# Kernel optimization log

Hardware: AMD Instinct MI355X
Metric: run time of the kernel (lower is better)

Reference implementation:

```python
import jax, jax.numpy as jnp
import numpy as np

N, F_IN, H1, H2, E = 100000, 256, 128, 64, 1600000


def _glorot(key, shape):
    lim = np.sqrt(6.0 / (shape[0] + shape[1]))
    return jax.random.uniform(key, shape, jnp.float32, -lim, lim)


def setup_inputs() -> dict:
    key = jax.random.key(0)
    ks = jax.random.split(key, 8)
    x = jax.random.normal(ks[0], (N, F_IN), jnp.float32)
    edge_index = jax.random.randint(ks[1], (2, E), 0, N, jnp.int64)
    return {
        "x": x,
        "w1": _glorot(ks[2], (F_IN, H1)),
        "b1": jnp.zeros((H1,), jnp.float32),
        "w2": _glorot(ks[3], (H1, H2)),
        "b2": jnp.zeros((H2,), jnp.float32),
        "w3": _glorot(ks[4], (H1, H2)),
        "b3": jnp.zeros((H2,), jnp.float32),
        "edge_index": edge_index,
    }


def _gcn_conv(x, w, b, src, dst, dinv_sqrt):
    # GCNConv: transform first, then symmetric-normalized aggregation with self-loops.
    h = x @ w                                   # [N, out]
    coef = dinv_sqrt[src] * dinv_sqrt[dst]      # [E]
    agg = jnp.zeros_like(h).at[dst].add(h[src] * coef[:, None])
    # self-loop contribution: coefficient deg^-1 per node
    agg = agg + h * (dinv_sqrt * dinv_sqrt)[:, None]
    return agg + b


def reference(x, w1, b1, w2, b2, w3, b3, edge_index):
    src, dst = edge_index[0], edge_index[1]
    n = x.shape[0]
    # degree including self-loop (edge weights all 1)
    deg = jnp.ones((n,), x.dtype).at[dst].add(1.0)
    dinv_sqrt = jax.lax.rsqrt(deg)
    hidden = jax.nn.relu(_gcn_conv(x, w1, b1, src, dst, dinv_sqrt))
    mu = _gcn_conv(hidden, w2, b2, src, dst, dinv_sqrt)
    logvar = _gcn_conv(hidden, w3, b3, src, dst, dinv_sqrt)
    return (mu, logvar)
```

## Files before the change

### kernel.cpp

```cpp
#include <hip/hip_runtime.h>


#define TPB 256
#define GSHIFT 9
#define GSIZE 512
#define PART_M 4096

typedef __attribute__((ext_vector_type(8))) short short8;
typedef __attribute__((ext_vector_type(4))) short short4v;
typedef __attribute__((ext_vector_type(4))) float floatx4;
typedef __attribute__((ext_vector_type(4))) unsigned int uint4v;

__device__ __forceinline__ void split2(float v, short& hi, short& lo) {
    unsigned u = __float_as_uint(v);
    float hf = __uint_as_float(u & 0xFFFF0000u);
    float lf = v - hf;
    hi = (short)(u >> 16);
    lo = (short)(__float_as_uint(lf) >> 16);
}

__device__ __forceinline__ short bf16_rtn(float v) {
    unsigned u = __float_as_uint(v);
    u += 0x7FFF + ((u >> 16) & 1);
    return (short)(u >> 16);
}

__device__ __forceinline__ void addrow(float* a, uint4v v) {
    a[0] += __uint_as_float(v[0] << 16); a[1] += __uint_as_float(v[0] & 0xFFFF0000u);
    a[2] += __uint_as_float(v[1] << 16); a[3] += __uint_as_float(v[1] & 0xFFFF0000u);
    a[4] += __uint_as_float(v[2] << 16); a[5] += __uint_as_float(v[2] & 0xFFFF0000u);
    a[6] += __uint_as_float(v[3] << 16); a[7] += __uint_as_float(v[3] & 0xFFFF0000u);
}

__device__ __forceinline__ void gather_accum(float* acc, const int* __restrict__ csr,
                                             int start, int deg, const uint4v* hp,
                                             int l16) {
    for (int jj = 0; jj < deg; jj += 16) {
        int rem = deg - jj;
        if (rem > 16) rem = 16;
        int il = (l16 < rem) ? l16 : rem - 1;
        int myIdx = csr[start + jj + il];
        int r = 0;
        for (; r + 3 < rem; r += 4) {
            int i0 = __shfl(myIdx, r + 0, 16);
            int i1 = __shfl(myIdx, r + 1, 16);
            int i2 = __shfl(myIdx, r + 2, 16);
            int i3 = __shfl(myIdx, r + 3, 16);
            uint4v v0 = hp[(size_t)i0 * 16 + l16];
            uint4v v1 = hp[(size_t)i1 * 16 + l16];
            uint4v v2 = hp[(size_t)i2 * 16 + l16];
            uint4v v3 = hp[(size_t)i3 * 16 + l16];
            addrow(acc, v0);
            addrow(acc, v1);
            addrow(acc, v2);
            addrow(acc, v3);
        }
        for (; r < rem; ++r) {
            int i = __shfl(myIdx, r, 16);
            addrow(acc, hp[(size_t)i * 16 + l16]);
        }
    }
}

__device__ __forceinline__ void gload_lds16(const void* g, void* l) {
    __builtin_amdgcn_global_load_lds(
        (const __attribute__((address_space(1))) unsigned int*)g,
        (__attribute__((address_space(3))) unsigned int*)l, 16, 0, 0);
}

__global__ __launch_bounds__(TPB) void prep_all(const float* __restrict__ w1,
                                                const float* __restrict__ w2,
                                                const float* __restrict__ b2,
                                                const float* __restrict__ w3,
                                                const float* __restrict__ b3,
                                                short* __restrict__ w1t_h,
                                                short* __restrict__ w1t_l,
                                                short* __restrict__ wct_h,
                                                short* __restrict__ wct_l,
                                                float* __restrict__ bcat,
                                                int* __restrict__ cursor) {
    int b = blockIdx.x, t0 = threadIdx.x;
    if (b < 128) {
        int t = b * TPB + t0;
        int k = t & 255, n = t >> 8;
        float v = w1[(size_t)k * 128 + n];
        short h, l;
        split2(v, h, l);
        w1t_h[t] = h;
        w1t_l[t] = l;
    } else if (b < 192) {
        int t = (b - 128) * TPB + t0;
        int k = t & 127, n = t >> 7;
        float v = (n < 64) ? w2[(size_t)k * 64 + n] : w3[(size_t)k * 64 + (n - 64)];
        short h, l;
        split2(v, h, l);
        wct_h[t] = h;
        wct_l[t] = l;
        if (t < 64) { bcat[t] = b2[t]; bcat[64 + t] = b3[t]; }
    } else {
        for (int i = t0; i < 513; i += TPB) cursor[i] = 0;
    }
}

__global__ __launch_bounds__(TPB) void group_count(const int* __restrict__ dst,
                                                   int* __restrict__ cursor, int E) {
    int* ghist = cursor;
    int* done  = cursor + 512;
    int* goff  = cursor + 513;
    __shared__ int h[256];
    __shared__ int lastFlag;
    int t = threadIdx.x;
    h[t] = 0;
    __syncthreads();
    const int4* d4 = (const int4*)dst;
    int E4 = E >> 2;
    int stride = gridDim.x * TPB;
    for (int k = blockIdx.x * TPB + t; k < E4; k += stride) {
        int4 v = d4[k];
        atomicAdd(&h[v.x >> GSHIFT], 1);
        atomicAdd(&h[v.y >> GSHIFT], 1);
        atomicAdd(&h[v.z >> GSHIFT], 1);
        atomicAdd(&h[v.w >> GSHIFT], 1);
    }
    for (int k = (E4 << 2) + blockIdx.x * TPB + t; k < E; k += stride)
        atomicAdd(&h[dst[k] >> GSHIFT], 1);
    __syncthreads();
    if (h[t]) atomicAdd(&ghist[t], h[t]);
    __threadfence();
    __syncthreads();
    if (t == 0) lastFlag = (atomicAdd(done, 1) == (int)gridDim.x - 1);
    __syncthreads();
    if (!lastFlag) return;
    int v = atomicAdd(&ghist[t], 0);
    h[t] = v;
    __syncthreads();
#pragma unroll
    for (int off = 1; off < 256; off <<= 1) {
        int x = (t >= off) ? h[t - off] : 0;
        __syncthreads();
        h[t] += x;
        __syncthreads();
    }
    goff[t] = h[t] - v;
    if (t == 255) goff[256] = h[255];
}

__global__ __launch_bounds__(256) void partition_kernel(const int* __restrict__ src,
                                                        const int* __restrict__ dst,
                                                        const int* __restrict__ goff,
                                                        int* __restrict__ gcur,
                                                        int* __restrict__ staged, int E) {
    __shared__ int sc[256];
    __shared__ int cur[256];
    __shared__ int gb[256];
    int t = threadIdx.x;
    int base = blockIdx.x * PART_M;
    int mloc = min(PART_M, E - base);
    int m4 = mloc >> 2;

    sc[t] = 0;
    cur[t] = 0;
    __syncthreads();
    const int4* d4 = (const int4*)(dst + base);
    const int4* s4 = (const int4*)(src + base);
    for (int k = t; k < m4; k += 256) {
        int4 v = d4[k];
        atomicAdd(&sc[v.x >> GSHIFT], 1);
        atomicAdd(&sc[v.y >> GSHIFT], 1);
        atomicAdd(&sc[v.z >> GSHIFT], 1);
        atomicAdd(&sc[v.w >> GSHIFT], 1);
    }
    for (int k = (m4 << 2) + t; k < mloc; k += 256)
        atomicAdd(&sc[dst[base + k] >> GSHIFT], 1);
    __syncthreads();
    int v = sc[t];
    gb[t] = v ? goff[t] + atomicAdd(&gcur[t], v) : 0;
    __syncthreads();
    for (int k = t; k < m4; k += 256) {
        int4 dv = d4[k];
        int4 sv = s4[k];
        int b0 = dv.x >> GSHIFT;
        staged[gb[b0] + atomicAdd(&cur[b0], 1)] = (sv.x << GSHIFT) | (dv.x & (GSIZE - 1));
        int b1 = dv.y >> GSHIFT;
        staged[gb[b1] + atomicAdd(&cur[b1], 1)] = (sv.y << GSHIFT) | (dv.y & (GSIZE - 1));
        int b2 = dv.z >> GSHIFT;
        staged[gb[b2] + atomicAdd(&cur[b2], 1)] = (sv.z << GSHIFT) | (dv.z & (GSIZE - 1));
        int b3 = dv.w >> GSHIFT;
        staged[gb[b3] + atomicAdd(&cur[b3], 1)] = (sv.w << GSHIFT) | (dv.w & (GSIZE - 1));
    }
    for (int k = (m4 << 2) + t; k < mloc; k += 256) {
        int d = dst[base + k];
        int s = src[base + k];
        int b = d >> GSHIFT;
        staged[gb[b] + atomicAdd(&cur[b], 1)] = (s << GSHIFT) | (d & (GSIZE - 1));
    }
}

__global__ __launch_bounds__(512) void build_csr(const int* __restrict__ staged,
                                                 const int* __restrict__ goff,
                                                 int* __restrict__ cnt,
                                                 float* __restrict__ dinv,
                                                 int* __restrict__ rowptr,
                                                 int* __restrict__ csr, int N) {
    __shared__ int hist[512];
    __shared__ int sc[512];
    __shared__ int lrow[512];
    __shared__ int cur[512];
    int t = threadIdx.x;
    int g = blockIdx.x;
    int s0 = goff[g], s1 = goff[g + 1];
    hist[t] = 0;
    cur[t] = 0;
    __syncthreads();
    for (int k = s0 + t; k < s1; k += 512)
        atomicAdd(&hist[staged[k] & (GSIZE - 1)], 1);
    __syncthreads();
    int v = hist[t];
    sc[t] = v;
    __syncthreads();
#pragma unroll
    for (int off = 1; off < 512; off <<= 1) {
        int x = (t >= off) ? sc[t - off] : 0;
        __syncthreads();
        sc[t] += x;
        __syncthreads();
    }
    int rp = s0 + sc[t] - v;
    lrow[t] = rp;
    int node = (g << GSHIFT) + t;
    if (node < N) {
        rowptr[node] = rp;
        cnt[node] = v;
        dinv[node] = rsqrtf(1.0f + (float)v);
    }
    __syncthreads();
    for (int k = s0 + t; k < s1; k += 512) {
        int p = staged[k];
        int dl = p & (GSIZE - 1);
        int pos = lrow[dl] + atomicAdd(&cur[dl], 1);
        csr[pos] = p >> GSHIFT;
    }
}

__global__ __launch_bounds__(TPB) void gemm_mfma_f32in(const float* __restrict__ A,
                                                       const short* __restrict__ Bth,
                                                       const short* __restrict__ Btl,
                                                       const float* __restrict__ rs,
                                                       short* __restrict__ Cb, int M, int K) {
    __shared__ float Af[2][64 * 32];
    __shared__ short Bh[2][128 * 32];
    __shared__ short Bl[2][128 * 32];
    int t = threadIdx.x;
    int wave = t >> 6, lane = t & 63, quad = lane >> 4, l16 = lane & 15;
    int bm0 = blockIdx.x * 64;

    floatx4 acc[8];
#pragma unroll
    for (int nt = 0; nt < 8; ++nt) acc[nt] = (floatx4){0.f, 0.f, 0.f, 0.f};

    auto stage = [&](int pb, int k0) {
#pragma unroll
        for (int i = 0; i < 2; ++i) {
            int g = i * 256 + t;
            int row = g >> 3, col = g & 7;
            int gr = bm0 + row;
            if (gr >= M) gr = M - 1;
            int scol = col ^ (row & 7);
            gload_lds16(A + (size_t)gr * K + k0 + scol * 4,
                        &Af[pb][(i * 256 + wave * 64) * 4]);
        }
#pragma unroll
        for (int i = 0; i < 2; ++i) {
            int g = i * 256 + t;
            int row = g >> 2, col = g & 3;
            int scol = col ^ ((row >> 1) & 3);
            size_t off = (size_t)row * K + k0 + scol * 8;
            int lb = (i * 256 + wave * 64) * 8;
            gload_lds16(Bth + off, &Bh[pb][lb]);
            gload_lds16(Btl + off, &Bl[pb][lb]);
        }
    };

    int nk = K >> 5;
    stage(0, 0);
    __syncthreads();
    int am = wave * 16 + l16;
    int ac0 = ((quad * 2 + 0) ^ (am & 7)) * 4;
    int ac1 = ((quad * 2 + 1) ^ (am & 7)) * 4;
    int bc = (quad ^ ((l16 >> 1) & 3)) * 8;
    for (int ks = 0; ks < nk; ++ks) {
        int pb = ks & 1;
        if (ks + 1 < nk) stage(pb ^ 1, (ks + 1) << 5);
        float4 fa0 = *(const float4*)&Af[pb][am * 32 + ac0];
        float4 fa1 = *(const float4*)&Af[pb][am * 32 + ac1];
        short8 a_h, a_l;
        {
            short h, l;
            split2(fa0.x, h, l); a_h[0] = h; a_l[0] = l;
            split2(fa0.y, h, l); a_h[1] = h; a_l[1] = l;
            split2(fa0.z, h, l); a_h[2] = h; a_l[2] = l;
            split2(fa0.w, h, l); a_h[3] = h; a_l[3] = l;
            split2(fa1.x, h, l); a_h[4] = h; a_l[4] = l;
            split2(fa1.y, h, l); a_h[5] = h; a_l[5] = l;
            split2(fa1.z, h, l); a_h[6] = h; a_l[6] = l;
            split2(fa1.w, h, l); a_h[7] = h; a_l[7] = l;
        }
#pragma unroll
        for (int nt = 0; nt < 8; ++nt) {
            int bn = nt * 16 + l16;
            short8 b_h = *(const short8*)&Bh[pb][bn * 32 + bc];
            short8 b_l = *(const short8*)&Bl[pb][bn * 32 + bc];
            acc[nt] = __builtin_amdgcn_mfma_f32_16x16x32_bf16(a_l, b_h, acc[nt], 0, 0, 0);
            acc[nt] = __builtin_amdgcn_mfma_f32_16x16x32_bf16(a_h, b_l, acc[nt], 0, 0, 0);
            acc[nt] = __builtin_amdgcn_mfma_f32_16x16x32_bf16(a_h, b_h, acc[nt], 0, 0, 0);
        }
        __syncthreads();
    }
#pragma unroll
    for (int reg = 0; reg < 4; ++reg) {
        int gr = bm0 + wave * 16 + quad * 4 + reg;
        if (gr < M) {
            float s = rs[gr];
            short* cp = Cb + (size_t)gr * 128;
#pragma unroll
            for (int nt = 0; nt < 8; ++nt) cp[nt * 16 + l16] = bf16_rtn(acc[nt][reg] * s);
        }
    }
}

__global__ __launch_bounds__(TPB) void gemm_mfma_bfin(const short* __restrict__ AH,
                                                      const short* __restrict__ AL,
                                                      const short* __restrict__ Bth,
                                                      const short* __restrict__ Btl,
                                                      const float* __restrict__ rs,
                                                      short* __restrict__ Cb, int M, int K) {
    __shared__ short Ah[2][64 * 32], Al[2][64 * 32];
    __shared__ short Bh[2][128 * 32], Bl[2][128 * 32];
    int t = threadIdx.x;
    int wave = t >> 6, lane = t & 63, quad = lane >> 4, l16 = lane & 15;
    int bm0 = blockIdx.x * 64;

    floatx4 acc[8];
#pragma unroll
    for (int nt = 0; nt < 8; ++nt) acc[nt] = (floatx4){0.f, 0.f, 0.f, 0.f};

    auto stage = [&](int pb, int k0) {
        {
            int row = t >> 2, col = t & 3;
            int gr = bm0 + row;
            if (gr >= M) gr = M - 1;
            int scol = col ^ ((row >> 1) & 3);
            size_t off = (size_t)gr * K + k0 + scol * 8;
            int lb = (wave * 64) * 8;
            gload_lds16(AH + off, &Ah[pb][lb]);
            gload_lds16(AL + off, &Al[pb][lb]);
        }
#pragma unroll
        for (int i = 0; i < 2; ++i) {
            int g = i * 256 + t;
            int row = g >> 2, col = g & 3;
            int scol = col ^ ((row >> 1) & 3);
            size_t off = (size_t)row * K + k0 + scol * 8;
            int lb = (i * 256 + wave * 64) * 8;
            gload_lds16(Bth + off, &Bh[pb][lb]);
            gload_lds16(Btl + off, &Bl[pb][lb]);
        }
    };

    int nk = K >> 5;
    stage(0, 0);
    __syncthreads();
    int am = wave * 16 + l16;
    int ac = (quad ^ ((am >> 1) & 3)) * 8;
    int bc = (quad ^ ((l16 >> 1) & 3)) * 8;
    for (int ks = 0; ks < nk; ++ks) {
        int pb = ks & 1;
        if (ks + 1 < nk) stage(pb ^ 1, (ks + 1) << 5);
        short8 a_h = *(const short8*)&Ah[pb][am * 32 + ac];
        short8 a_l = *(const short8*)&Al[pb][am * 32 + ac];
#pragma unroll
        for (int nt = 0; nt < 8; ++nt) {
            int bn = nt * 16 + l16;
            short8 b_h = *(const short8*)&Bh[pb][bn * 32 + bc];
            short8 b_l = *(const short8*)&Bl[pb][bn * 32 + bc];
            acc[nt] = __builtin_amdgcn_mfma_f32_16x16x32_bf16(a_l, b_h, acc[nt], 0, 0, 0);
            acc[nt] = __builtin_amdgcn_mfma_f32_16x16x32_bf16(a_h, b_l, acc[nt], 0, 0, 0);
            acc[nt] = __builtin_amdgcn_mfma_f32_16x16x32_bf16(a_h, b_h, acc[nt], 0, 0, 0);
        }
        __syncthreads();
    }
#pragma unroll
    for (int reg = 0; reg < 4; ++reg) {
        int gr = bm0 + wave * 16 + quad * 4 + reg;
        if (gr < M) {
            float s = rs[gr];
            short* cp = Cb + (size_t)gr * 128;
#pragma unroll
            for (int nt = 0; nt < 8; ++nt) cp[nt * 16 + l16] = bf16_rtn(acc[nt][reg] * s);
        }
    }
}

__global__ __launch_bounds__(TPB) void gather_hidden(const int* __restrict__ csr,
                                                     const int* __restrict__ rowptr,
                                                     const int* __restrict__ cnt,
                                                     const float* __restrict__ dinv,
                                                     const short* __restrict__ hs,
                                                     const float* __restrict__ b1,
                                                     short* __restrict__ hidH,
                                                     short* __restrict__ hidL, int N) {
    size_t t = (size_t)blockIdx.x * TPB + threadIdx.x;
    int nid = (int)(t >> 4);
    int lane = threadIdx.x & 15;
    if (nid >= N) return;
    int start = rowptr[nid];
    int deg = cnt[nid];
    const uint4v* hp = (const uint4v*)hs;
    float acc[8] = {0, 0, 0, 0, 0, 0, 0, 0};
    addrow(acc, __builtin_nontemporal_load(&hp[(size_t)nid * 16 + lane]));
    gather_accum(acc, csr, start, deg, hp, lane);
    float di = dinv[nid];
    float4 b0 = ((const float4*)b1)[lane * 2];
    float4 b1v = ((const float4*)b1)[lane * 2 + 1];
    float bb[8] = {b0.x, b0.y, b0.z, b0.w, b1v.x, b1v.y, b1v.z, b1v.w};
    unsigned hiw[8];
    short low[8];
#pragma unroll
    for (int i = 0; i < 8; ++i) {
        float h = fmaxf(fmaf(di, acc[i], bb[i]), 0.f);
        unsigned u = __float_as_uint(h);
        hiw[i] = u >> 16;
        float hf = __uint_as_float(u & 0xFFFF0000u);
        low[i] = bf16_rtn(h - hf);
    }
    uint4v ph, pl;
    ph[0] = hiw[0] | (hiw[1] << 16);
    ph[1] = hiw[2] | (hiw[3] << 16);
    ph[2] = hiw[4] | (hiw[5] << 16);
    ph[3] = hiw[6] | (hiw[7] << 16);
    pl[0] = (unsigned short)low[0] | ((unsigned)(unsigned short)low[1] << 16);
    pl[1] = (unsigned short)low[2] | ((unsigned)(unsigned short)low[3] << 16);
    pl[2] = (unsigned short)low[4] | ((unsigned)(unsigned short)low[5] << 16);
    pl[3] = (unsigned short)low[6] | ((unsigned)(unsigned short)low[7] << 16);
    __builtin_nontemporal_store(ph, &((uint4v*)hidH)[(size_t)nid * 16 + lane]);
    __builtin_nontemporal_store(pl, &((uint4v*)hidL)[(size_t)nid * 16 + lane]);
}

__global__ __launch_bounds__(TPB) void gather_out(const int* __restrict__ csr,
                                                  const int* __restrict__ rowptr,
                                                  const int* __restrict__ cnt,
                                                  const float* __restrict__ dinv,
                                                  const short* __restrict__ hs,
                                                  const float* __restrict__ bcat,
                                                  float* __restrict__ out, int N) {
    size_t t = (size_t)blockIdx.x * TPB + threadIdx.x;
    int nid = (int)(t >> 4);
    int lane = threadIdx.x & 15;
    if (nid >= N) return;
    int start = rowptr[nid];
    int deg = cnt[nid];
    const uint4v* hp = (const uint4v*)hs;
    float acc[8] = {0, 0, 0, 0, 0, 0, 0, 0};
    addrow(acc, __builtin_nontemporal_load(&hp[(size_t)nid * 16 + lane]));
    gather_accum(acc, csr, start, deg, hp, lane);
    float di = dinv[nid];
    float4 b0 = ((const float4*)bcat)[lane * 2];
    float4 b1v = ((const float4*)bcat)[lane * 2 + 1];
    floatx4 r0, r1;
    r0[0] = fmaf(di, acc[0], b0.x);
    r0[1] = fmaf(di, acc[1], b0.y);
    r0[2] = fmaf(di, acc[2], b0.z);
    r0[3] = fmaf(di, acc[3], b0.w);
    r1[0] = fmaf(di, acc[4], b1v.x);
    r1[1] = fmaf(di, acc[5], b1v.y);
    r1[2] = fmaf(di, acc[6], b1v.z);
    r1[3] = fmaf(di, acc[7], b1v.w);
    int f = lane * 8;
    float* dp = (f < 64) ? (out + (size_t)nid * 64 + f)
                         : (out + (size_t)N * 64 + (size_t)nid * 64 + (f - 64));
    __builtin_nontemporal_store(r0, (floatx4*)dp);
    __builtin_nontemporal_store(r1, (floatx4*)(dp + 4));
}

extern "C" void kernel_launch(void* const* d_in, const int* in_sizes, int n_in,
                              void* d_out, int out_size, void* d_ws, size_t ws_size,
                              hipStream_t stream) {
    const float* x  = (const float*)d_in[0];
    const float* w1 = (const float*)d_in[1];
    const float* b1 = (const float*)d_in[2];
    const float* w2 = (const float*)d_in[3];
    const float* b2 = (const float*)d_in[4];
    const float* w3 = (const float*)d_in[5];
    const float* b3 = (const float*)d_in[6];
    const int*   ei = (const int*)d_in[7];

    const int N = in_sizes[0] / 256;
    const int E = in_sizes[7] / 2;
    const int K1 = 256;

    float* out = (float*)d_out;

    size_t nh = (size_t)N * 128;
    short* hs1    = (short*)d_ws;
    short* hidH   = hs1 + nh;
    short* hidL   = hidH + nh;
    short* hs2    = hidL + nh;
    int*   cnt    = (int*)(hs2 + nh);
    float* dinv   = (float*)(cnt + N);
    int*   rowptr = (int*)(dinv + N);
    int*   cursor = rowptr + N;
    int*   bsum   = cursor + N;
    float* bcat   = (float*)(bsum + 512);
    short* w1t_h  = (short*)(bcat + 128);
    short* w1t_l  = w1t_h + 128 * 256;
    short* wct_h  = w1t_l + 128 * 256;
    short* wct_l  = wct_h + 128 * 128;
    int*   csr    = (int*)(wct_l + 128 * 128);

    const int* srcp = ei;
    const int* dstp = ei + E;

    const int ngrp = (N + GSIZE - 1) >> GSHIFT;
    int* gcur   = cursor + 256;
    int* goff   = cursor + 513;
    int* staged = (int*)hs2;

    prep_all<<<193, TPB, 0, stream>>>(w1, w2, b2, w3, b3, w1t_h, w1t_l, wct_h, wct_l,
                                      bcat, cursor);

    int gc_blocks = ((E >> 2) + TPB * 4 - 1) / (TPB * 4);
    group_count<<<gc_blocks, TPB, 0, stream>>>(dstp, cursor, E);
    partition_kernel<<<(E + PART_M - 1) / PART_M, 256, 0, stream>>>(srcp, dstp, goff, gcur,
                                                                    staged, E);
    build_csr<<<ngrp, 512, 0, stream>>>(staged, goff, cnt, dinv, rowptr, csr, N);

    gemm_mfma_f32in<<<(N + 63) / 64, TPB, 0, stream>>>(x, w1t_h, w1t_l, dinv, hs1, N, K1);

    size_t gthreads = (size_t)N * 16;
    gather_hidden<<<(unsigned)((gthreads + TPB - 1) / TPB), TPB, 0, stream>>>(
        csr, rowptr, cnt, dinv, hs1, b1, hidH, hidL, N);

    gemm_mfma_bfin<<<(N + 63) / 64, TPB, 0, stream>>>(hidH, hidL, wct_h, wct_l, dinv, hs2, N, 128);

    gather_out<<<(unsigned)((gthreads + TPB - 1) / TPB), TPB, 0, stream>>>(
        csr, rowptr, cnt, dinv, hs2, bcat, out, N);
}
```

Baseline: 412.7 us.

## Double M tile in both MFMA GEMMs and drop nontemporal hints in gathers

Both split-bf16 GEMM kernels now compute 128 rows per block instead of 64, with each wave handling two 16-row M subtiles. Every B fragment read from LDS is therefore reused across two A subtiles, which halves B staging traffic per output row and the number of blocks launched. In exchange, LDS use and accumulator registers per wave roughly double, which can lower occupancy. Separately, the gather kernels switch their self-row loads and hidden-layer stores from nontemporal to ordinary accesses, so the intermediate hidden arrays can stay in cache for the next GEMM.

```diff
diff --git a/kernel.cpp b/kernel.cpp
--- a/kernel.cpp
+++ b/kernel.cpp
@@ -247,20 +247,22 @@
                                                        const short* __restrict__ Btl,
                                                        const float* __restrict__ rs,
                                                        short* __restrict__ Cb, int M, int K) {
-    __shared__ float Af[2][64 * 32];
+    __shared__ float Af[2][128 * 32];
     __shared__ short Bh[2][128 * 32];
     __shared__ short Bl[2][128 * 32];
     int t = threadIdx.x;
     int wave = t >> 6, lane = t & 63, quad = lane >> 4, l16 = lane & 15;
-    int bm0 = blockIdx.x * 64;
-
-    floatx4 acc[8];
-#pragma unroll
-    for (int nt = 0; nt < 8; ++nt) acc[nt] = (floatx4){0.f, 0.f, 0.f, 0.f};
+    int bm0 = blockIdx.x * 128;
+
+    floatx4 acc[2][8];
+#pragma unroll
+    for (int mt = 0; mt < 2; ++mt)
+#pragma unroll
+        for (int nt = 0; nt < 8; ++nt) acc[mt][nt] = (floatx4){0.f, 0.f, 0.f, 0.f};
 
     auto stage = [&](int pb, int k0) {
 #pragma unroll
-        for (int i = 0; i < 2; ++i) {
+        for (int i = 0; i < 4; ++i) {
             int g = i * 256 + t;
             int row = g >> 3, col = g & 7;
             int gr = bm0 + row;
@@ -284,48 +286,55 @@
     int nk = K >> 5;
     stage(0, 0);
     __syncthreads();
-    int am = wave * 16 + l16;
-    int ac0 = ((quad * 2 + 0) ^ (am & 7)) * 4;
-    int ac1 = ((quad * 2 + 1) ^ (am & 7)) * 4;
+    int r0 = wave * 32 + l16;
+    int ac0 = ((quad * 2 + 0) ^ (r0 & 7)) * 4;
+    int ac1 = ((quad * 2 + 1) ^ (r0 & 7)) * 4;
     int bc = (quad ^ ((l16 >> 1) & 3)) * 8;
     for (int ks = 0; ks < nk; ++ks) {
         int pb = ks & 1;
         if (ks + 1 < nk) stage(pb ^ 1, (ks + 1) << 5);
-        float4 fa0 = *(const float4*)&Af[pb][am * 32 + ac0];
-        float4 fa1 = *(const float4*)&Af[pb][am * 32 + ac1];
-        short8 a_h, a_l;
-        {
+        short8 a_h[2], a_l[2];
+#pragma unroll
+        for (int mt = 0; mt < 2; ++mt) {
+            int r = r0 + mt * 16;
+            float4 fa0 = *(const float4*)&Af[pb][r * 32 + ac0];
+            float4 fa1 = *(const float4*)&Af[pb][r * 32 + ac1];
             short h, l;
-            split2(fa0.x, h, l); a_h[0] = h; a_l[0] = l;
-            split2(fa0.y, h, l); a_h[1] = h; a_l[1] = l;
-            split2(fa0.z, h, l); a_h[2] = h; a_l[2] = l;
-            split2(fa0.w, h, l); a_h[3] = h; a_l[3] = l;
-            split2(fa1.x, h, l); a_h[4] = h; a_l[4] = l;
-            split2(fa1.y, h, l); a_h[5] = h; a_l[5] = l;
-            split2(fa1.z, h, l); a_h[6] = h; a_l[6] = l;
-            split2(fa1.w, h, l); a_h[7] = h; a_l[7] = l;
+            split2(fa0.x, h, l); a_h[mt][0] = h; a_l[mt][0] = l;
+            split2(fa0.y, h, l); a_h[mt][1] = h; a_l[mt][1] = l;
+            split2(fa0.z, h, l); a_h[mt][2] = h; a_l[mt][2] = l;
+            split2(fa0.w, h, l); a_h[mt][3] = h; a_l[mt][3] = l;
+            split2(fa1.x, h, l); a_h[mt][4] = h; a_l[mt][4] = l;
+            split2(fa1.y, h, l); a_h[mt][5] = h; a_l[mt][5] = l;
+            split2(fa1.z, h, l); a_h[mt][6] = h; a_l[mt][6] = l;
+            split2(fa1.w, h, l); a_h[mt][7] = h; a_l[mt][7] = l;
         }
 #pragma unroll
         for (int nt = 0; nt < 8; ++nt) {
             int bn = nt * 16 + l16;
             short8 b_h = *(const short8*)&Bh[pb][bn * 32 + bc];
             short8 b_l = *(const short8*)&Bl[pb][bn * 32 + bc];
-            acc[nt] = __builtin_amdgcn_mfma_f32_16x16x32_bf16(a_l, b_h, acc[nt], 0, 0, 0);
-            acc[nt] = __builtin_amdgcn_mfma_f32_16x16x32_bf16(a_h, b_l, acc[nt], 0, 0, 0);
-            acc[nt] = __builtin_amdgcn_mfma_f32_16x16x32_bf16(a_h, b_h, acc[nt], 0, 0, 0);
+#pragma unroll
+            for (int mt = 0; mt < 2; ++mt) {
+                acc[mt][nt] = __builtin_amdgcn_mfma_f32_16x16x32_bf16(a_l[mt], b_h, acc[mt][nt], 0, 0, 0);
+                acc[mt][nt] = __builtin_amdgcn_mfma_f32_16x16x32_bf16(a_h[mt], b_l, acc[mt][nt], 0, 0, 0);
+                acc[mt][nt] = __builtin_amdgcn_mfma_f32_16x16x32_bf16(a_h[mt], b_h, acc[mt][nt], 0, 0, 0);
+            }
         }
         __syncthreads();
     }
 #pragma unroll
-    for (int reg = 0; reg < 4; ++reg) {
-        int gr = bm0 + wave * 16 + quad * 4 + reg;
-        if (gr < M) {
-            float s = rs[gr];
-            short* cp = Cb + (size_t)gr * 128;
-#pragma unroll
-            for (int nt = 0; nt < 8; ++nt) cp[nt * 16 + l16] = bf16_rtn(acc[nt][reg] * s);
-        }
-    }
+    for (int mt = 0; mt < 2; ++mt)
+#pragma unroll
+        for (int reg = 0; reg < 4; ++reg) {
+            int gr = bm0 + wave * 32 + mt * 16 + quad * 4 + reg;
+            if (gr < M) {
+                float s = rs[gr];
+                short* cp = Cb + (size_t)gr * 128;
+#pragma unroll
+                for (int nt = 0; nt < 8; ++nt) cp[nt * 16 + l16] = bf16_rtn(acc[mt][nt][reg] * s);
+            }
+        }
 }
 
 __global__ __launch_bounds__(TPB) void gemm_mfma_bfin(const short* __restrict__ AH,
@@ -334,24 +343,28 @@
                                                       const short* __restrict__ Btl,
                                                       const float* __restrict__ rs,
                                                       short* __restrict__ Cb, int M, int K) {
-    __shared__ short Ah[2][64 * 32], Al[2][64 * 32];
+    __shared__ short Ah[2][128 * 32], Al[2][128 * 32];
     __shared__ short Bh[2][128 * 32], Bl[2][128 * 32];
     int t = threadIdx.x;
     int wave = t >> 6, lane = t & 63, quad = lane >> 4, l16 = lane & 15;
-    int bm0 = blockIdx.x * 64;
-
-    floatx4 acc[8];
-#pragma unroll
-    for (int nt = 0; nt < 8; ++nt) acc[nt] = (floatx4){0.f, 0.f, 0.f, 0.f};
+    int bm0 = blockIdx.x * 128;
+
+    floatx4 acc[2][8];
+#pragma unroll
+    for (int mt = 0; mt < 2; ++mt)
+#pragma unroll
+        for (int nt = 0; nt < 8; ++nt) acc[mt][nt] = (floatx4){0.f, 0.f, 0.f, 0.f};
 
     auto stage = [&](int pb, int k0) {
-        {
-            int row = t >> 2, col = t & 3;
+#pragma unroll
+        for (int i = 0; i < 2; ++i) {
+            int g = i * 256 + t;
+            int row = g >> 2, col = g & 3;
             int gr = bm0 + row;
             if (gr >= M) gr = M - 1;
             int scol = col ^ ((row >> 1) & 3);
             size_t off = (size_t)gr * K + k0 + scol * 8;
-            int lb = (wave * 64) * 8;
+            int lb = (i * 256 + wave * 64) * 8;
             gload_lds16(AH + off, &Ah[pb][lb]);
             gload_lds16(AL + off, &Al[pb][lb]);
         }
@@ -370,35 +383,45 @@
     int nk = K >> 5;
     stage(0, 0);
     __syncthreads();
-    int am = wave * 16 + l16;
-    int ac = (quad ^ ((am >> 1) & 3)) * 8;
+    int r0 = wave * 32 + l16;
+    int ac = (quad ^ ((r0 >> 1) & 3)) * 8;
     int bc = (quad ^ ((l16 >> 1) & 3)) * 8;
     for (int ks = 0; ks < nk; ++ks) {
         int pb = ks & 1;
         if (ks + 1 < nk) stage(pb ^ 1, (ks + 1) << 5);
-        short8 a_h = *(const short8*)&Ah[pb][am * 32 + ac];
-        short8 a_l = *(const short8*)&Al[pb][am * 32 + ac];
+        short8 a_h[2], a_l[2];
+#pragma unroll
+        for (int mt = 0; mt < 2; ++mt) {
+            int r = r0 + mt * 16;
+            a_h[mt] = *(const short8*)&Ah[pb][r * 32 + ac];
+            a_l[mt] = *(const short8*)&Al[pb][r * 32 + ac];
+        }
 #pragma unroll
         for (int nt = 0; nt < 8; ++nt) {
             int bn = nt * 16 + l16;
             short8 b_h = *(const short8*)&Bh[pb][bn * 32 + bc];
             short8 b_l = *(const short8*)&Bl[pb][bn * 32 + bc];
-            acc[nt] = __builtin_amdgcn_mfma_f32_16x16x32_bf16(a_l, b_h, acc[nt], 0, 0, 0);
-            acc[nt] = __builtin_amdgcn_mfma_f32_16x16x32_bf16(a_h, b_l, acc[nt], 0, 0, 0);
-            acc[nt] = __builtin_amdgcn_mfma_f32_16x16x32_bf16(a_h, b_h, acc[nt], 0, 0, 0);
+#pragma unroll
+            for (int mt = 0; mt < 2; ++mt) {
+                acc[mt][nt] = __builtin_amdgcn_mfma_f32_16x16x32_bf16(a_l[mt], b_h, acc[mt][nt], 0, 0, 0);
+                acc[mt][nt] = __builtin_amdgcn_mfma_f32_16x16x32_bf16(a_h[mt], b_l, acc[mt][nt], 0, 0, 0);
+                acc[mt][nt] = __builtin_amdgcn_mfma_f32_16x16x32_bf16(a_h[mt], b_h, acc[mt][nt], 0, 0, 0);
+            }
         }
         __syncthreads();
     }
 #pragma unroll
-    for (int reg = 0; reg < 4; ++reg) {
-        int gr = bm0 + wave * 16 + quad * 4 + reg;
-        if (gr < M) {
-            float s = rs[gr];
-            short* cp = Cb + (size_t)gr * 128;
-#pragma unroll
-            for (int nt = 0; nt < 8; ++nt) cp[nt * 16 + l16] = bf16_rtn(acc[nt][reg] * s);
-        }
-    }
+    for (int mt = 0; mt < 2; ++mt)
+#pragma unroll
+        for (int reg = 0; reg < 4; ++reg) {
+            int gr = bm0 + wave * 32 + mt * 16 + quad * 4 + reg;
+            if (gr < M) {
+                float s = rs[gr];
+                short* cp = Cb + (size_t)gr * 128;
+#pragma unroll
+                for (int nt = 0; nt < 8; ++nt) cp[nt * 16 + l16] = bf16_rtn(acc[mt][nt][reg] * s);
+            }
+        }
 }
 
 __global__ __launch_bounds__(TPB) void gather_hidden(const int* __restrict__ csr,
@@ -417,7 +440,7 @@
     int deg = cnt[nid];
     const uint4v* hp = (const uint4v*)hs;
     float acc[8] = {0, 0, 0, 0, 0, 0, 0, 0};
-    addrow(acc, __builtin_nontemporal_load(&hp[(size_t)nid * 16 + lane]));
+    addrow(acc, hp[(size_t)nid * 16 + lane]);
     gather_accum(acc, csr, start, deg, hp, lane);
     float di = dinv[nid];
     float4 b0 = ((const float4*)b1)[lane * 2];
@@ -442,8 +465,8 @@
     pl[1] = (unsigned short)low[2] | ((unsigned)(unsigned short)low[3] << 16);
     pl[2] = (unsigned short)low[4] | ((unsigned)(unsigned short)low[5] << 16);
     pl[3] = (unsigned short)low[6] | ((unsigned)(unsigned short)low[7] << 16);
-    __builtin_nontemporal_store(ph, &((uint4v*)hidH)[(size_t)nid * 16 + lane]);
-    __builtin_nontemporal_store(pl, &((uint4v*)hidL)[(size_t)nid * 16 + lane]);
+    ((uint4v*)hidH)[(size_t)nid * 16 + lane] = ph;
+    ((uint4v*)hidL)[(size_t)nid * 16 + lane] = pl;
 }
 
 __global__ __launch_bounds__(TPB) void gather_out(const int* __restrict__ csr,
@@ -461,7 +484,7 @@
     int deg = cnt[nid];
     const uint4v* hp = (const uint4v*)hs;
     float acc[8] = {0, 0, 0, 0, 0, 0, 0, 0};
-    addrow(acc, __builtin_nontemporal_load(&hp[(size_t)nid * 16 + lane]));
+    addrow(acc, hp[(size_t)nid * 16 + lane]);
     gather_accum(acc, csr, start, deg, hp, lane);
     float di = dinv[nid];
     float4 b0 = ((const float4*)bcat)[lane * 2];
@@ -534,13 +557,13 @@
                                                                     staged, E);
     build_csr<<<ngrp, 512, 0, stream>>>(staged, goff, cnt, dinv, rowptr, csr, N);
 
-    gemm_mfma_f32in<<<(N + 63) / 64, TPB, 0, stream>>>(x, w1t_h, w1t_l, dinv, hs1, N, K1);
+    gemm_mfma_f32in<<<(N + 127) / 128, TPB, 0, stream>>>(x, w1t_h, w1t_l, dinv, hs1, N, K1);
 
     size_t gthreads = (size_t)N * 16;
     gather_hidden<<<(unsigned)((gthreads + TPB - 1) / TPB), TPB, 0, stream>>>(
         csr, rowptr, cnt, dinv, hs1, b1, hidH, hidL, N);
 
-    gemm_mfma_bfin<<<(N + 63) / 64, TPB, 0, stream>>>(hidH, hidL, wct_h, wct_l, dinv, hs2, N, 128);
+    gemm_mfma_bfin<<<(N + 127) / 128, TPB, 0, stream>>>(hidH, hidL, wct_h, wct_l, dinv, hs2, N, 128);
 
     gather_out<<<(unsigned)((gthreads + TPB - 1) / TPB), TPB, 0, stream>>>(
         csr, rowptr, cnt, dinv, hs2, bcat, out, N);
```

Result: no change. 406.8 us (-1.4%).
